# Performance work log

Measured on AMD Instinct MI355X. Metric: run time of the kernel, lower is better.

Reference implementation:

```python
import jax, jax.numpy as jnp
import numpy as np
from jax import lax

K = 20
ALPHA = 0.1
N_NODES = 100000
N_EDGES = 3200000


def setup_inputs() -> dict:
    key = jax.random.key(0)
    k1, k2, k3, k4, k5, k6 = jax.random.split(key, 6)
    x = jax.random.normal(k1, (N_NODES, 512), dtype=jnp.float32)
    edge_index = jax.random.randint(k2, (2, N_EDGES), 0, N_NODES, dtype=jnp.int32)
    W1 = jax.random.normal(k3, (512, 128), dtype=jnp.float32) * 0.05
    b1 = jax.random.normal(k4, (128,), dtype=jnp.float32) * 0.05
    W2 = jax.random.normal(k5, (128, 40), dtype=jnp.float32) * 0.05
    b2 = jax.random.normal(k6, (40,), dtype=jnp.float32) * 0.05
    return {"x": x, "edge_index": edge_index, "W1": W1, "b1": b1, "W2": W2, "b2": b2}


def reference(x, edge_index, W1, b1, W2, b2):
    N = x.shape[0]
    # MLP encoder (dropout is identity in eval mode)
    h = jax.nn.relu(x @ W1 + b1)          # [N, 128]
    h = jax.nn.relu(h @ W2 + b2)          # [N, num_classes]

    # gcn_norm with self-loops (PyG APPNP default: normalize=True, add_self_loops=True)
    loop = jnp.arange(N, dtype=edge_index.dtype)
    row = jnp.concatenate([edge_index[0], loop])  # source nodes
    col = jnp.concatenate([edge_index[1], loop])  # target nodes
    deg = jax.ops.segment_sum(jnp.ones_like(col, dtype=h.dtype), col, num_segments=N)
    dinv = jnp.where(deg > 0, lax.rsqrt(deg), 0.0)
    norm = dinv[row] * dinv[col]          # [E + N]

    h0 = h

    def step(z, _):
        msg = norm[:, None] * z[row]                       # gather + scale
        agg = jax.ops.segment_sum(msg, col, num_segments=N)  # scatter-add
        z = (1.0 - ALPHA) * agg + ALPHA * h0
        return z, None

    z, _ = lax.scan(step, h0, None, length=K)
    return z
```

## Files before the change

kernel.cpp:

```cpp
#include <hip/hip_runtime.h>
#include <hip/hip_bf16.h>

#define K_ITERS 20
#define F_IN 512
#define F_HID 128
#define F_OUT 40
#define SCAN_CHUNK 512


__global__ void k_hist(const int* __restrict__ col, int E, int* __restrict__ cnt){
  int e = blockIdx.x*blockDim.x + threadIdx.x;
  if (e < E) atomicAdd(&cnt[col[e]], 1);
}

__global__ void k_dinv(const int* __restrict__ cnt, int N, float* __restrict__ dinv){
  int i = blockIdx.x*blockDim.x + threadIdx.x;
  if (i < N) dinv[i] = rsqrtf((float)(cnt[i] + 1));
}

__global__ void k_scan1(const int* __restrict__ cnt, int N, int* __restrict__ bsum){
  __shared__ int sd[256];
  int base = blockIdx.x * SCAN_CHUNK;
  int t = threadIdx.x;
  int i0 = base + 2*t, i1 = i0+1;
  int s = ((i0<N)?cnt[i0]:0) + ((i1<N)?cnt[i1]:0);
  sd[t] = s; __syncthreads();
  for (int off=1; off<256; off<<=1){
    int v = (t>=off)? sd[t-off] : 0;
    __syncthreads();
    sd[t] += v;
    __syncthreads();
  }
  if (t==255) bsum[blockIdx.x] = sd[255];
}
__global__ void k_scan2(const int* __restrict__ bsum, int NB, int* __restrict__ boff,
                        int* __restrict__ row_ptr, int N, int E){
  __shared__ int sd[256];
  int t = threadIdx.x;
  int v = (t < NB) ? bsum[t] : 0;
  sd[t] = v; __syncthreads();
  for (int off=1; off<256; off<<=1){
    int u = (t>=off)? sd[t-off] : 0;
    __syncthreads();
    sd[t] += u;
    __syncthreads();
  }
  if (t < NB) boff[t] = sd[t] - v;
  if (t == 0) row_ptr[N] = E;
}
__global__ void k_scan3(const int* __restrict__ cnt, int N, const int* __restrict__ boff,
                        int* __restrict__ row_ptr){
  __shared__ int sd[256];
  int base = blockIdx.x * SCAN_CHUNK;
  int t = threadIdx.x;
  int i0 = base + 2*t, i1 = i0+1;
  int c0 = (i0<N)?cnt[i0]:0, c1 = (i1<N)?cnt[i1]:0;
  int s = c0+c1;
  sd[t] = s; __syncthreads();
  for (int off=1; off<256; off<<=1){
    int v = (t>=off)? sd[t-off] : 0;
    __syncthreads();
    sd[t] += v;
    __syncthreads();
  }
  int excl = sd[t] - s + boff[blockIdx.x];
  if (i0<N) row_ptr[i0] = excl;
  if (i1<N) row_ptr[i1] = excl + c0;
}

__global__ void k_scatter(const int* __restrict__ row, const int* __restrict__ col, int E,
                          const int* __restrict__ row_ptr, int* __restrict__ cur,
                          const float* __restrict__ dinv,
                          int* __restrict__ csr_src, float* __restrict__ csr_norm){
  int e = blockIdx.x*blockDim.x + threadIdx.x;
  if (e >= E) return;
  int r = row[e], c = col[e];
  int p = row_ptr[c] + atomicAdd(&cur[c], 1);
  csr_src[p] = r;
  csr_norm[p] = dinv[r]*dinv[c];
}

__global__ __launch_bounds__(256) void k_mlp(const float* __restrict__ x,
                      const float* __restrict__ W1, const float* __restrict__ b1,
                      const float* __restrict__ W2, const float* __restrict__ b2,
                      float* __restrict__ h0, int N){
  __shared__ float h1t[16][F_HID];
  __shared__ float w2s[F_HID*F_OUT];
  __shared__ float b2s[F_OUT];
  const int t   = threadIdx.x;
  const int hid = t & 127;
  const int half = __builtin_amdgcn_readfirstlane(t >> 7);
  const int nb  = blockIdx.x * 16;

  for (int i = t; i < F_HID*F_OUT; i += 256) w2s[i] = W2[i];
  if (t < F_OUT) b2s[t] = b2[t];

  const float* rp[8];
  #pragma unroll
  for (int n = 0; n < 8; n++){
    int r = nb + half*8 + n;
    if (r >= N) r = N - 1;
    rp[n] = x + (size_t)r * F_IN;
  }

  float acc[8];
  const float bb = b1[hid];
  #pragma unroll
  for (int n = 0; n < 8; n++) acc[n] = bb;

  #pragma unroll 4
  for (int k = 0; k < F_IN; k++){
    const float w = W1[k*F_HID + hid];
    #pragma unroll
    for (int n = 0; n < 8; n++) acc[n] += rp[n][k] * w;
  }

  #pragma unroll
  for (int n = 0; n < 8; n++) h1t[half*8 + n][hid] = fmaxf(acc[n], 0.f);
  __syncthreads();

  for (int i = t; i < 16*F_OUT; i += 256){
    const int node = i / F_OUT, c = i - node*F_OUT;
    float a = b2s[c];
    #pragma unroll 4
    for (int k = 0; k < F_HID; k++)
      a += h1t[node][k] * w2s[k*F_OUT + c];
    const int gn = nb + node;
    if (gn < N) h0[(size_t)gn*F_OUT + c] = fmaxf(a, 0.f);
  }
}

__global__ __launch_bounds__(64) void k_prop(const int* __restrict__ row_ptr, const int* __restrict__ csr_src,
                      const float* __restrict__ csr_norm, const float* __restrict__ dinv,
                      const float* __restrict__ zin, const float* __restrict__ h0,
                      float* __restrict__ zout, int N){
  const int node = blockIdx.x;
  const int lane = threadIdx.x;
  if (lane >= F_OUT) return;
  const int beg = row_ptr[node], end = row_ptr[node+1];
  float acc = 0.f;
  int p = beg;

  int   cs[8]; float cn[8];
  bool have = (p + 8 <= end);
  if (have){
    #pragma unroll
    for (int j = 0; j < 8; j++){ cs[j] = csr_src[p+j]; cn[j] = csr_norm[p+j]; }
  }
  while (have){
    const int np = p + 8;
    const bool nh = (np + 8 <= end);
    int ns[8]; float nn[8];
    if (nh){
      #pragma unroll
      for (int j = 0; j < 8; j++){ ns[j] = csr_src[np+j]; nn[j] = csr_norm[np+j]; }
    }
    float z[8];
    #pragma unroll
    for (int j = 0; j < 8; j++) z[j] = zin[(size_t)cs[j]*F_OUT + lane];
    #pragma unroll
    for (int j = 0; j < 8; j++) acc += cn[j]*z[j];
    p = np; have = nh;
    if (nh){
      #pragma unroll
      for (int j = 0; j < 8; j++){ cs[j] = ns[j]; cn[j] = nn[j]; }
    }
  }
  for (; p < end; ++p)
    acc += csr_norm[p] * zin[(size_t)csr_src[p]*F_OUT + lane];

  const float di = dinv[node];
  const size_t idx = (size_t)node*F_OUT + lane;
  acc += di*di*zin[idx];
  zout[idx] = 0.9f*acc + 0.1f*h0[idx];
}

extern "C" void kernel_launch(void* const* d_in, const int* in_sizes, int n_in,
                              void* d_out, int out_size, void* d_ws, size_t ws_size,
                              hipStream_t stream){
  const float* x  = (const float*)d_in[0];
  const int*   ei = (const int*)d_in[1];
  const float* W1 = (const float*)d_in[2];
  const float* b1 = (const float*)d_in[3];
  const float* W2 = (const float*)d_in[4];
  const float* b2 = (const float*)d_in[5];
  int N = in_sizes[0] / F_IN;
  int E = in_sizes[1] / 2;
  const int* row = ei;
  const int* col = ei + E;

  char* w = (char*)d_ws;
  auto alloc = [&](size_t bytes)->void*{ void* p = w; w += (bytes + 255) & ~255ull; return p; };
  int*   cnt      = (int*)  alloc((size_t)N*4);
  int*   cur      = (int*)  alloc((size_t)N*4);
  int*   row_ptr  = (int*)  alloc(((size_t)N+1)*4);
  float* dinv     = (float*)alloc((size_t)N*4);
  int NB = (N + SCAN_CHUNK-1)/SCAN_CHUNK;
  int*   bsum     = (int*)  alloc((size_t)NB*4);
  int*   boff     = (int*)  alloc((size_t)NB*4);
  int*   csr_src  = (int*)  alloc((size_t)E*4);
  float* csr_norm = (float*)alloc((size_t)E*4);
  float* h0       = (float*)alloc((size_t)N*F_OUT*4);
  float* zA       = (float*)alloc((size_t)N*F_OUT*4);
  float* zB       = (float*)alloc((size_t)N*F_OUT*4);

  (void)hipMemsetAsync(cnt, 0, (size_t)N*4, stream);
  (void)hipMemsetAsync(cur, 0, (size_t)N*4, stream);

  int ge = (E + 255)/256;
  k_hist   <<<ge, 256, 0, stream>>>(col, E, cnt);
  k_dinv   <<<(N+255)/256, 256, 0, stream>>>(cnt, N, dinv);
  k_scan1  <<<NB, 256, 0, stream>>>(cnt, N, bsum);
  k_scan2  <<<1, 256, 0, stream>>>(bsum, NB, boff, row_ptr, N, E);
  k_scan3  <<<NB, 256, 0, stream>>>(cnt, N, boff, row_ptr);
  k_scatter<<<ge, 256, 0, stream>>>(row, col, E, row_ptr, cur, dinv, csr_src, csr_norm);

  k_mlp<<<(N+15)/16, 256, 0, stream>>>(x, W1, b1, W2, b2, h0, N);

  float* zi = h0; float* zo = zA;
  for (int it=0; it<K_ITERS; ++it){
    float* dst = (it == K_ITERS-1) ? (float*)d_out : zo;
    k_prop<<<N, 64, 0, stream>>>(row_ptr, csr_src, csr_norm, dinv, zi, h0, dst, N);
    float* nxt = (it==0) ? zB : zi;
    zi = zo; zo = nxt;
  }
}
```

Measured before the change: 3.207 ms.

## Register-tile MLP with LDS double-buffered W1 and pack four nodes per prop block

The MLP kernel is rewritten so each block handles 64 nodes, with each thread computing an 8x4 register tile. W1 tiles are staged into LDS through async global_load_lds with double buffering, and x is read as float4. The second layer now assigns 10 output columns per wave and reads from a transposed LDS buffer. The propagation kernel packs four nodes into a 256-thread block instead of one node per 64-thread block, which cuts block count and scheduling overhead at the cost of some idle lanes per wave.

```diff
diff --git a/kernel.cpp b/kernel.cpp
--- a/kernel.cpp
+++ b/kernel.cpp
@@ -7,6 +7,9 @@
 #define F_OUT 40
 #define SCAN_CHUNK 512
 
+
+typedef const float __attribute__((address_space(1)))* glb_fp;
+typedef float __attribute__((address_space(3)))* lds_fp;
 
 __global__ void k_hist(const int* __restrict__ col, int E, int* __restrict__ cnt){
   int e = blockIdx.x*blockDim.x + threadIdx.x;
@@ -84,58 +87,107 @@
                       const float* __restrict__ W1, const float* __restrict__ b1,
                       const float* __restrict__ W2, const float* __restrict__ b2,
                       float* __restrict__ h0, int N){
-  __shared__ float h1t[16][F_HID];
-  __shared__ float w2s[F_HID*F_OUT];
-  __shared__ float b2s[F_OUT];
-  const int t   = threadIdx.x;
-  const int hid = t & 127;
-  const int half = __builtin_amdgcn_readfirstlane(t >> 7);
-  const int nb  = blockIdx.x * 16;
-
-  for (int i = t; i < F_HID*F_OUT; i += 256) w2s[i] = W2[i];
-  if (t < F_OUT) b2s[t] = b2[t];
-
-  const float* rp[8];
+  __shared__ float lds[8704];
+  const int t    = threadIdx.x;
+  const int th   = t & 31;
+  const int tn   = t >> 5;
+  const int lane = t & 63;
+  const int wv   = __builtin_amdgcn_readfirstlane(t >> 6);
+  const int nb   = blockIdx.x * 64;
+
+  const float* xp[8];
   #pragma unroll
-  for (int n = 0; n < 8; n++){
-    int r = nb + half*8 + n;
-    if (r >= N) r = N - 1;
-    rp[n] = x + (size_t)r * F_IN;
-  }
-
-  float acc[8];
-  const float bb = b1[hid];
+  for (int j=0;j<8;++j){
+    int r = nb + tn*8 + j; if (r >= N) r = N-1;
+    const float* p = x + (size_t)r * F_IN;
+    asm volatile("" : "+v"(p));
+    xp[j] = p;
+  }
+
+  auto stage = [&](int kt, int b){
+    const float* gs = W1 + kt*(32*128) + wv*1024 + lane*4;
+    int lo = __builtin_amdgcn_readfirstlane((b*4096 + wv*1024) * 4);
+    #pragma unroll
+    for (int i=0;i<4;++i){
+      __builtin_amdgcn_global_load_lds((glb_fp)(gs + i*256),
+        (lds_fp)((char*)lds + lo + i*1024), 16, 0, 0);
+    }
+  };
+
+  float acc[8][4];
+  {
+    float4 bb = *(const float4*)(b1 + th*4);
+    #pragma unroll
+    for (int j=0;j<8;++j){ acc[j][0]=bb.x; acc[j][1]=bb.y; acc[j][2]=bb.z; acc[j][3]=bb.w; }
+  }
+
+  stage(0, 0);
+  __syncthreads();
+
+  for (int kt=0; kt<16; ++kt){
+    const int cur = kt & 1;
+    if (kt < 15) stage(kt+1, cur^1);
+    const int kbase = kt*32;
+    #pragma unroll
+    for (int c=0;c<8;++c){
+      const int kb = kbase + c*4;
+      float4 xv[8];
+      #pragma unroll
+      for (int j=0;j<8;++j) xv[j] = *(const float4*)(xp[j] + kb);
+      const float* wl = lds + cur*4096 + c*512 + th*4;
+      float4 wa = *(const float4*)(wl);
+      float4 wb = *(const float4*)(wl + 128);
+      float4 wc = *(const float4*)(wl + 256);
+      float4 wd = *(const float4*)(wl + 384);
+      #pragma unroll
+      for (int j=0;j<8;++j){
+        acc[j][0] += xv[j].x*wa.x; acc[j][1] += xv[j].x*wa.y; acc[j][2] += xv[j].x*wa.z; acc[j][3] += xv[j].x*wa.w;
+        acc[j][0] += xv[j].y*wb.x; acc[j][1] += xv[j].y*wb.y; acc[j][2] += xv[j].y*wb.z; acc[j][3] += xv[j].y*wb.w;
+        acc[j][0] += xv[j].z*wc.x; acc[j][1] += xv[j].z*wc.y; acc[j][2] += xv[j].z*wc.z; acc[j][3] += xv[j].z*wc.w;
+        acc[j][0] += xv[j].w*wd.x; acc[j][1] += xv[j].w*wd.y; acc[j][2] += xv[j].w*wd.z; acc[j][3] += xv[j].w*wd.w;
+      }
+    }
+    __syncthreads();
+  }
+
   #pragma unroll
-  for (int n = 0; n < 8; n++) acc[n] = bb;
-
+  for (int h=0; h<4; ++h){
+    const int hid = th*4 + h;
+    float4 v0 = make_float4(fmaxf(acc[0][h],0.f), fmaxf(acc[1][h],0.f),
+                            fmaxf(acc[2][h],0.f), fmaxf(acc[3][h],0.f));
+    float4 v1 = make_float4(fmaxf(acc[4][h],0.f), fmaxf(acc[5][h],0.f),
+                            fmaxf(acc[6][h],0.f), fmaxf(acc[7][h],0.f));
+    *(float4*)&lds[hid*68 + tn*8]     = v0;
+    *(float4*)&lds[hid*68 + tn*8 + 4] = v1;
+  }
+  __syncthreads();
+
+  const int c0 = wv*10;
+  float a2[10];
+  #pragma unroll
+  for (int i=0;i<10;++i) a2[i] = b2[c0+i];
   #pragma unroll 4
-  for (int k = 0; k < F_IN; k++){
-    const float w = W1[k*F_HID + hid];
-    #pragma unroll
-    for (int n = 0; n < 8; n++) acc[n] += rp[n][k] * w;
-  }
-
-  #pragma unroll
-  for (int n = 0; n < 8; n++) h1t[half*8 + n][hid] = fmaxf(acc[n], 0.f);
-  __syncthreads();
-
-  for (int i = t; i < 16*F_OUT; i += 256){
-    const int node = i / F_OUT, c = i - node*F_OUT;
-    float a = b2s[c];
-    #pragma unroll 4
-    for (int k = 0; k < F_HID; k++)
-      a += h1t[node][k] * w2s[k*F_OUT + c];
-    const int gn = nb + node;
-    if (gn < N) h0[(size_t)gn*F_OUT + c] = fmaxf(a, 0.f);
-  }
-}
-
-__global__ __launch_bounds__(64) void k_prop(const int* __restrict__ row_ptr, const int* __restrict__ csr_src,
+  for (int k=0;k<F_HID;++k){
+    const float hv = lds[k*68 + lane];
+    #pragma unroll
+    for (int i=0;i<10;++i) a2[i] += hv * W2[k*F_OUT + c0 + i];
+  }
+  const int gn = nb + lane;
+  if (gn < N){
+    float* o = h0 + (size_t)gn*F_OUT + c0;
+    #pragma unroll
+    for (int i=0;i<10;++i) o[i] = fmaxf(a2[i], 0.f);
+  }
+}
+
+__global__ __launch_bounds__(256) void k_prop(const int* __restrict__ row_ptr, const int* __restrict__ csr_src,
                       const float* __restrict__ csr_norm, const float* __restrict__ dinv,
                       const float* __restrict__ zin, const float* __restrict__ h0,
                       float* __restrict__ zout, int N){
-  const int node = blockIdx.x;
-  const int lane = threadIdx.x;
+  const int wv   = __builtin_amdgcn_readfirstlane((int)(threadIdx.x >> 6));
+  const int node = blockIdx.x*4 + wv;
+  const int lane = threadIdx.x & 63;
+  if (node >= N) return;
   if (lane >= F_OUT) return;
   const int beg = row_ptr[node], end = row_ptr[node+1];
   float acc = 0.f;
@@ -215,12 +267,13 @@
   k_scan3  <<<NB, 256, 0, stream>>>(cnt, N, boff, row_ptr);
   k_scatter<<<ge, 256, 0, stream>>>(row, col, E, row_ptr, cur, dinv, csr_src, csr_norm);
 
-  k_mlp<<<(N+15)/16, 256, 0, stream>>>(x, W1, b1, W2, b2, h0, N);
+  k_mlp<<<(N+63)/64, 256, 0, stream>>>(x, W1, b1, W2, b2, h0, N);
 
   float* zi = h0; float* zo = zA;
+  int gp = (N + 3)/4;
   for (int it=0; it<K_ITERS; ++it){
     float* dst = (it == K_ITERS-1) ? (float*)d_out : zo;
-    k_prop<<<N, 64, 0, stream>>>(row_ptr, csr_src, csr_norm, dinv, zi, h0, dst, N);
+    k_prop<<<gp, 256, 0, stream>>>(row_ptr, csr_src, csr_norm, dinv, zi, h0, dst, N);
     float* nxt = (it==0) ? zB : zi;
     zi = zo; zo = nxt;
   }
```

Measured after the change: 2.851 ms. 11.1% less time.
